# Kernel optimization log

Hardware: AMD Instinct MI355X
Metric: run time of the kernel (lower is better)

Reference implementation:

```python
import jax, jax.numpy as jnp
import numpy as np
import math

N_EMBD = 1024
N_HEAD = 16
HEAD_DIM = N_EMBD // N_HEAD


def setup_inputs() -> dict:
    key = jax.random.key(0)
    k_x, k_w1, k_b1, k_w2, k_b2 = jax.random.split(key, 5)
    B, T = 2, 2048
    x = jax.random.normal(k_x, (B, T, N_EMBD), dtype=jnp.float32)
    # ln1: Linear(n_embd, 3*n_embd); weights stored as [in, out] for x @ W
    W_qkv = jax.random.normal(k_w1, (N_EMBD, 3 * N_EMBD), dtype=jnp.float32) * 0.02
    b_qkv = jax.random.normal(k_b1, (3 * N_EMBD,), dtype=jnp.float32) * 0.02
    # ln2: Linear(n_embd, n_embd)
    W_out = jax.random.normal(k_w2, (N_EMBD, N_EMBD), dtype=jnp.float32) * 0.02
    b_out = jax.random.normal(k_b2, (N_EMBD,), dtype=jnp.float32) * 0.02
    return {"x": x, "W_qkv": W_qkv, "b_qkv": b_qkv, "W_out": W_out, "b_out": b_out}


def reference(x, W_qkv, b_qkv, W_out, b_out):
    B, T, C = x.shape
    qkv = x @ W_qkv + b_qkv                      # [B,T,3C]
    q, k, v = jnp.split(qkv, 3, axis=-1)
    # reshape to heads: [B, H, T, D]
    def to_heads(t):
        return t.reshape(B, T, N_HEAD, HEAD_DIM).transpose(0, 2, 1, 3)
    Q, K, V = to_heads(q), to_heads(k), to_heads(v)
    # NOTE: scale is 1/sqrt(n_head), as in the source (not sqrt(head_dim));
    # NOTE: no causal mask is applied, faithfully matching the source forward.
    scale = 1.0 / math.sqrt(N_HEAD)
    scores = jnp.einsum('bhqd,bhkd->bhqk', Q, K) * scale  # [B,H,T,T]
    attn = jax.nn.softmax(scores, axis=-1)
    out = jnp.einsum('bhqk,bhkd->bhqd', attn, V)          # [B,H,T,D]
    out = out.transpose(0, 2, 1, 3).reshape(B, T, C)
    # dropout = 0.0 -> identity (eval mode)
    return out @ W_out + b_out
```

## Files before the change

kernel.cpp:

```cpp
#include <hip/hip_runtime.h>
#include <hip/hip_bf16.h>
#include <stdint.h>

typedef __bf16 bf16_t;
typedef __bf16 bf16x8 __attribute__((ext_vector_type(8)));
typedef float  f32x4  __attribute__((ext_vector_type(4)));

#define AS1 __attribute__((address_space(1)))
#define AS3 __attribute__((address_space(3)))

__device__ __forceinline__ void gload16(const bf16_t* g, char* l) {
  __builtin_amdgcn_global_load_lds((AS1 const void*)(uintptr_t)g, (AS3 void*)l, 16, 0, 0);
}
__device__ __forceinline__ int swz8(int r) { return (r & 7) ^ ((r >> 2) & 6); }

#define C2S 0.36067376022224085f

__global__ __launch_bounds__(256) void prep(
    const float* __restrict__ x, const float* __restrict__ Wqkv, const float* __restrict__ Wout,
    bf16_t* __restrict__ xb, bf16_t* __restrict__ wqkvT, bf16_t* __restrict__ woutT) {
  __shared__ float tile[32][33];
  const int bid = blockIdx.x, tid = threadIdx.x;
  if (bid < 4096) {
    const int i = bid * 256 + tid;
    float4 v = reinterpret_cast<const float4*>(x)[i];
    union { bf16_t h[4]; unsigned long long u; } r;
    r.h[0] = (bf16_t)v.x; r.h[1] = (bf16_t)v.y; r.h[2] = (bf16_t)v.z; r.h[3] = (bf16_t)v.w;
    reinterpret_cast<unsigned long long*>(xb)[i] = r.u;
    return;
  }
  const float* W; bf16_t* Wt; int N, tb;
  if (bid < 7168) { W = Wqkv; Wt = wqkvT; N = 3072; tb = bid - 4096; }
  else            { W = Wout; Wt = woutT; N = 1024; tb = bid - 7168; }
  const int kb = (tb & 31) * 32, nb = (tb >> 5) * 32;
  const int tx = tid & 31, ty = tid >> 5;
#pragma unroll
  for (int i = 0; i < 32; i += 8)
    tile[ty + i][tx] = W[(size_t)(kb + ty + i) * N + nb + tx];
  __syncthreads();
  const int r = tid >> 3;
  const int c0 = (tid & 7) * 4;
  union { bf16_t h4[4]; unsigned long long u; } pk;
#pragma unroll
  for (int j = 0; j < 4; ++j) pk.h4[j] = (bf16_t)tile[c0 + j][r];
  *reinterpret_cast<unsigned long long*>(&Wt[(size_t)(nb + r) * 1024 + kb + c0]) = pk.u;
}

__global__ __launch_bounds__(512) void gemm8(
    const bf16_t* __restrict__ A, const bf16_t* __restrict__ Bt,
    const float* __restrict__ bias,
    bf16_t* __restrict__ outb, bf16_t* __restrict__ vtb,
    int N, int K, int ldo) {
  __shared__ bf16_t lA[3][4096];
  __shared__ bf16_t lB[3][4096];
  const int tid = threadIdx.x;
  const int wave = tid >> 6, lane = tid & 63;
  const int lr = lane & 15, lg = lane >> 4;
  const int ntiles = N >> 7;
  const int bid = (blockIdx.x & 7) * ((int)gridDim.x >> 3) + (blockIdx.x >> 3);
  const int bn = bid % ntiles, bm = bid / ntiles;
  const int m0 = bm * 128, n0 = bn * 128;
  const int wr = wave >> 2, wc = wave & 3;
  f32x4 acc[4][2] = {};

  const int srow = tid >> 2;
  const int scolb = ((tid & 3) << 4) ^ (((srow >> 1) & 3) << 4);
  const bf16_t* Asrc = A  + (size_t)(m0 + srow) * K + (scolb >> 1);
  const bf16_t* Bsrc = Bt + (size_t)(n0 + srow) * K + (scolb >> 1);
  auto stage = [&](int buf, int k0) {
    gload16(Asrc + k0, (char*)&lA[buf][0] + wave * 1024);
    gload16(Bsrc + k0, (char*)&lB[buf][0] + wave * 1024);
  };

  auto ldA = [&](const char* p, int mi) {
    const int row = wr * 64 + mi * 16 + lr;
    return *reinterpret_cast<const bf16x8*>(p + row * 64 + ((lg * 16) ^ (((row >> 1) & 3) << 4)));
  };
  auto ldB = [&](const char* p, int ni) {
    const int row = wc * 32 + ni * 16 + lr;
    return *reinterpret_cast<const bf16x8*>(p + row * 64 + ((lg * 16) ^ (((row >> 1) & 3) << 4)));
  };

  const int nt = K >> 5;
  stage(0, 0);
  stage(1, 32);
  int cur = 0, stg = 2;

  for (int t = 0; t < nt; ++t) {
    if (t + 2 < nt) {
      stage(stg, (t + 2) << 5);
      asm volatile("s_waitcnt vmcnt(4)" ::: "memory");
    } else if (t + 1 < nt) {
      asm volatile("s_waitcnt vmcnt(2)" ::: "memory");
    } else {
      asm volatile("s_waitcnt vmcnt(0)" ::: "memory");
    }
    __builtin_amdgcn_s_barrier();
    __builtin_amdgcn_sched_barrier(0);

    const char* pA = (const char*)&lA[cur][0];
    const char* pB = (const char*)&lB[cur][0];
    bf16x8 af[4], bfv[2];
#pragma unroll
    for (int mi = 0; mi < 4; ++mi) af[mi] = ldA(pA, mi);
    bfv[0] = ldB(pB, 0); bfv[1] = ldB(pB, 1);

    __builtin_amdgcn_s_setprio(1);
#pragma unroll
    for (int mi = 0; mi < 4; ++mi)
#pragma unroll
      for (int ni = 0; ni < 2; ++ni)
        acc[mi][ni] = __builtin_amdgcn_mfma_f32_16x16x32_bf16(af[mi], bfv[ni], acc[mi][ni], 0, 0, 0);
    __builtin_amdgcn_s_setprio(0);

    __builtin_amdgcn_sched_barrier(0);
    __builtin_amdgcn_s_barrier();
    cur = cur == 2 ? 0 : cur + 1;
    stg = stg == 2 ? 0 : stg + 1;
  }

#pragma unroll
  for (int mi = 0; mi < 4; ++mi) {
#pragma unroll
    for (int ni = 0; ni < 2; ++ni) {
      const int col = n0 + wc * 32 + ni * 16 + lr;
      const float bv = bias[col];
      const int rg0 = m0 + wr * 64 + mi * 16 + lg * 4;
      if (col >= 2048) {
        const int colv = col - 2048;
        const int dd = colv & 63, hh = colv >> 6;
        const int bb = rg0 >> 11, t = rg0 & 2047;
        union { bf16_t h4[4]; unsigned long long u; } pk;
#pragma unroll
        for (int r = 0; r < 4; ++r) pk.h4[r] = (bf16_t)(acc[mi][ni][r] + bv);
        *reinterpret_cast<unsigned long long*>(
            vtb + (size_t)(bb * 16 + hh) * 131072 + (size_t)dd * 2048 + t) = pk.u;
      } else {
        const float sc = (col < 1024) ? C2S : 1.f;
#pragma unroll
        for (int r = 0; r < 4; ++r) {
          const float v = (acc[mi][ni][r] + bv) * sc;
          outb[(size_t)(rg0 + r) * ldo + col] = (bf16_t)v;
        }
      }
    }
  }
}

__global__ __launch_bounds__(512) void attn_fwd(
    const bf16_t* __restrict__ qkv2,
    const bf16_t* __restrict__ vT,
    bf16_t* __restrict__ a0, bf16_t* __restrict__ a1,
    float* __restrict__ lbuf) {
  __shared__ bf16_t lds[3][8192];
  const int tid = threadIdx.x;
  const int wave = tid >> 6, lane = tid & 63;
  const int lr = lane & 15, lg = lane >> 4;
  const int id = blockIdx.x;
  const int xcd = id & 7, slot = id >> 3;
  const int bh = xcd * 4 + (slot & 3);
  const int rest = slot >> 2;
  const int qb = rest & 7, kvh = rest >> 3;
  const int b = bh >> 4, h = bh & 15;

  const int q0 = qb * 256 + wave * 32;
  const bf16_t* Qp = qkv2 + (size_t)(b * 2048 + q0) * 2048 + h * 64;
  bf16x8 qf[2][2];
#pragma unroll
  for (int hx = 0; hx < 2; ++hx) {
    qf[hx][0] = *reinterpret_cast<const bf16x8*>(Qp + (size_t)(hx * 16 + lr) * 2048 + lg * 8);
    qf[hx][1] = *reinterpret_cast<const bf16x8*>(Qp + (size_t)(hx * 16 + lr) * 2048 + 32 + lg * 8);
  }

  const int kr = tid >> 3;
  const int ks = (tid & 7) ^ swz8(kr);
  const bf16_t* Ksrc = qkv2 + (size_t)(b * 2048 + kvh * 1024 + kr) * 2048 + 1024 + h * 64 + ks * 8;
  const bf16_t* Vsrc = vT + (size_t)bh * 131072 + (size_t)kr * 2048 + kvh * 1024 + ks * 8;

  auto stage = [&](int buf, int kb) {
    char* base = (char*)&lds[buf][0] + wave * 1024;
    gload16(Ksrc + (size_t)kb * 131072, base);
    gload16(Vsrc + (size_t)kb * 64, base + 8192);
  };

  int kofs[4][2], vofs[4][2];
#pragma unroll
  for (int t = 0; t < 4; ++t) {
    const int kk = 32 * (t >> 1) + 8 * (lr >> 2) + 4 * (t & 1) + (lr & 3);
    const int sw = swz8(kk) << 4;
    kofs[t][0] = (kk << 7) + ((lg * 16) ^ sw);
    kofs[t][1] = (kk << 7) + ((64 + lg * 16) ^ sw);
  }
#pragma unroll
  for (int nc = 0; nc < 4; ++nc) {
    const int vr = nc * 16 + lr;
    const int sw = swz8(vr) << 4;
    vofs[nc][0] = 8192 + (vr << 7) + ((lg * 16) ^ sw);
    vofs[nc][1] = 8192 + (vr << 7) + ((64 + lg * 16) ^ sw);
  }

  f32x4 acc[2][4] = {};
  f32x4 accl[2] = {};
  bf16x8 ones;
#pragma unroll
  for (int j = 0; j < 8; ++j) ones[j] = (bf16_t)1.0f;

  stage(0, 0);
  stage(1, 1);
  int cur = 0, stg = 2;

  for (int kb = 0; kb < 16; ++kb) {
    if (kb + 2 < 16) stage(stg, kb + 2);
    if (kb + 2 < 16)      asm volatile("s_waitcnt vmcnt(4)" ::: "memory");
    else if (kb + 1 < 16) asm volatile("s_waitcnt vmcnt(2)" ::: "memory");
    else                  asm volatile("s_waitcnt vmcnt(0)" ::: "memory");
    __builtin_amdgcn_s_barrier();
    __builtin_amdgcn_sched_barrier(0);
    const char* bK = (const char*)&lds[cur][0];

    f32x4 s[2][4];
#pragma unroll
    for (int t = 0; t < 4; ++t) {
      const bf16x8 k0 = *reinterpret_cast<const bf16x8*>(bK + kofs[t][0]);
      const bf16x8 k1 = *reinterpret_cast<const bf16x8*>(bK + kofs[t][1]);
#pragma unroll
      for (int hx = 0; hx < 2; ++hx) {
        f32x4 z = {0.f, 0.f, 0.f, 0.f};
        z = __builtin_amdgcn_mfma_f32_16x16x32_bf16(k0, qf[hx][0], z, 0, 0, 0);
        s[hx][t] = __builtin_amdgcn_mfma_f32_16x16x32_bf16(k1, qf[hx][1], z, 0, 0, 0);
      }
    }

    bf16x8 pa[2][2];
#pragma unroll
    for (int hx = 0; hx < 2; ++hx) {
      float p[16];
#pragma unroll
      for (int t = 0; t < 4; ++t)
#pragma unroll
        for (int r = 0; r < 4; ++r)
          p[t * 4 + r] = __builtin_amdgcn_exp2f(s[hx][t][r]);
#pragma unroll
      for (int j = 0; j < 8; ++j) { pa[hx][0][j] = (bf16_t)p[j]; pa[hx][1][j] = (bf16_t)p[8 + j]; }
    }

    __builtin_amdgcn_s_setprio(1);
#pragma unroll
    for (int hx = 0; hx < 2; ++hx) {
      accl[hx] = __builtin_amdgcn_mfma_f32_16x16x32_bf16(pa[hx][0], ones, accl[hx], 0, 0, 0);
      accl[hx] = __builtin_amdgcn_mfma_f32_16x16x32_bf16(pa[hx][1], ones, accl[hx], 0, 0, 0);
    }
#pragma unroll
    for (int nc = 0; nc < 4; ++nc) {
      const bf16x8 v0 = *reinterpret_cast<const bf16x8*>(bK + vofs[nc][0]);
      const bf16x8 v1 = *reinterpret_cast<const bf16x8*>(bK + vofs[nc][1]);
#pragma unroll
      for (int hx = 0; hx < 2; ++hx) {
        acc[hx][nc] = __builtin_amdgcn_mfma_f32_16x16x32_bf16(pa[hx][0], v0, acc[hx][nc], 0, 0, 0);
        acc[hx][nc] = __builtin_amdgcn_mfma_f32_16x16x32_bf16(pa[hx][1], v1, acc[hx][nc], 0, 0, 0);
      }
    }
    __builtin_amdgcn_s_setprio(0);

    __builtin_amdgcn_sched_barrier(0);
    __builtin_amdgcn_s_barrier();
    cur = cur == 2 ? 0 : cur + 1;
    stg = stg == 2 ? 0 : stg + 1;
  }

  bf16_t* ap = kvh ? a1 : a0;
#pragma unroll
  for (int hx = 0; hx < 2; ++hx) {
#pragma unroll
    for (int r = 0; r < 4; ++r) {
      const float lf = 1.f / accl[hx][r];
      const int qg = q0 + hx * 16 + lg * 4 + r;
      bf16_t* op = ap + (size_t)(b * 2048 + qg) * 1024 + h * 64 + lr;
#pragma unroll
      for (int nc = 0; nc < 4; ++nc) op[nc * 16] = (bf16_t)(acc[hx][nc][r] * lf);
      if (lr == 0)
        lbuf[(size_t)(kvh * 4096 + b * 2048 + qg) * 16 + h] = accl[hx][r];
    }
  }
}

__global__ __launch_bounds__(256) void gemm2m(
    const bf16_t* __restrict__ a0, const bf16_t* __restrict__ a1,
    const float* __restrict__ lbuf, const bf16_t* __restrict__ Bt,
    const float* __restrict__ bias, float* __restrict__ outf) {
  __shared__ bf16_t lA[2][2048];
  __shared__ bf16_t lB[2][4096];
  const int tid = threadIdx.x;
  const int wave = tid >> 6, lane = tid & 63;
  const int lr = lane & 15, lg = lane >> 4;
  const int bid = (blockIdx.x & 7) * 64 + (blockIdx.x >> 3);
  const int bm = bid >> 3, bn = bid & 7;
  const int m0 = bm * 64, n0 = bn * 128;
  const int wr = wave >> 1, wc = wave & 1;
  f32x4 acc[2][4] = {};

  const int srow = tid >> 2;
  const int scolb = ((tid & 3) << 4) ^ (((srow >> 1) & 3) << 4);
  const int scol = scolb >> 1;

  const bf16_t* pa0 = a0 + (size_t)(m0 + srow) * 1024 + scol;
  const bf16_t* pa1 = a1 + (size_t)(m0 + srow) * 1024 + scol;
  const float*  pl0 = lbuf + (size_t)(m0 + srow) * 16;
  const float*  pl1 = lbuf + (size_t)(4096 + m0 + srow) * 16;
  const bf16_t* pB0 = Bt + (size_t)(n0 + srow) * 1024 + scol;
  const bf16_t* pB1 = Bt + (size_t)(n0 + 64 + srow) * 1024 + scol;

  bf16x8 nA0 = *reinterpret_cast<const bf16x8*>(pa0);
  bf16x8 nA1 = *reinterpret_cast<const bf16x8*>(pa1);
  float  nl0 = pl0[0], nl1 = pl1[0];
  bf16x8 nB0v = *reinterpret_cast<const bf16x8*>(pB0);
  bf16x8 nB1v = *reinterpret_cast<const bf16x8*>(pB1);

  for (int t = 0; t < 32; ++t) {
    const int cur = t & 1;
    const float inv = 1.f / (nl0 + nl1);
    const float w0 = nl0 * inv, w1 = nl1 * inv;
    bf16x8 mv;
#pragma unroll
    for (int j = 0; j < 8; ++j)
      mv[j] = (bf16_t)(w0 * (float)nA0[j] + w1 * (float)nA1[j]);
    *reinterpret_cast<bf16x8*>((char*)&lA[cur][0] + tid * 16) = mv;
    *reinterpret_cast<bf16x8*>((char*)&lB[cur][0] + tid * 16) = nB0v;
    *reinterpret_cast<bf16x8*>((char*)&lB[cur][0] + 4096 + tid * 16) = nB1v;
    __syncthreads();

    if (t < 31) {
      const int k0 = (t + 1) * 32;
      const int h = k0 >> 6;
      nA0 = *reinterpret_cast<const bf16x8*>(pa0 + k0);
      nA1 = *reinterpret_cast<const bf16x8*>(pa1 + k0);
      nl0 = pl0[h]; nl1 = pl1[h];
      nB0v = *reinterpret_cast<const bf16x8*>(pB0 + k0);
      nB1v = *reinterpret_cast<const bf16x8*>(pB1 + k0);
    }

    const char* pA = (const char*)&lA[cur][0];
    const char* pB = (const char*)&lB[cur][0];
    bf16x8 af[2], bfv[4];
#pragma unroll
    for (int mi = 0; mi < 2; ++mi) {
      const int row = wr * 32 + mi * 16 + lr;
      af[mi] = *reinterpret_cast<const bf16x8*>(pA + row * 64 + ((lg * 16) ^ (((row >> 1) & 3) << 4)));
    }
#pragma unroll
    for (int ni = 0; ni < 4; ++ni) {
      const int row = wc * 64 + ni * 16 + lr;
      bfv[ni] = *reinterpret_cast<const bf16x8*>(pB + row * 64 + ((lg * 16) ^ (((row >> 1) & 3) << 4)));
    }
    __builtin_amdgcn_s_setprio(1);
#pragma unroll
    for (int mi = 0; mi < 2; ++mi)
#pragma unroll
      for (int ni = 0; ni < 4; ++ni)
        acc[mi][ni] = __builtin_amdgcn_mfma_f32_16x16x32_bf16(af[mi], bfv[ni], acc[mi][ni], 0, 0, 0);
    __builtin_amdgcn_s_setprio(0);
    __syncthreads();
  }

#pragma unroll
  for (int mi = 0; mi < 2; ++mi)
#pragma unroll
    for (int ni = 0; ni < 4; ++ni) {
      const int col = n0 + wc * 64 + ni * 16 + lr;
      const float bv = bias[col];
      const int rg0 = m0 + wr * 32 + mi * 16 + lg * 4;
#pragma unroll
      for (int r = 0; r < 4; ++r)
        outf[(size_t)(rg0 + r) * 1024 + col] = acc[mi][ni][r] + bv;
    }
}

extern "C" void kernel_launch(void* const* d_in, const int* in_sizes, int n_in,
                              void* d_out, int out_size, void* d_ws, size_t ws_size,
                              hipStream_t stream) {
  (void)in_sizes; (void)n_in; (void)out_size; (void)ws_size;
  const float* x    = (const float*)d_in[0];
  const float* Wqkv = (const float*)d_in[1];
  const float* bqkv = (const float*)d_in[2];
  const float* Wout = (const float*)d_in[3];
  const float* bout = (const float*)d_in[4];
  float* out = (float*)d_out;

  char* ws = (char*)d_ws;
  bf16_t* xb    = (bf16_t*)(ws);
  bf16_t* a0    = (bf16_t*)(ws);
  bf16_t* wqkvT = (bf16_t*)(ws + 8388608);
  bf16_t* woutT = (bf16_t*)(ws + 14680064);
  bf16_t* qkv2  = (bf16_t*)(ws + 16777216);
  bf16_t* vT    = (bf16_t*)(ws + 33554432);
  bf16_t* a1    = (bf16_t*)(ws + 41943040);
  float*  lbuf  = (float*)(ws + 50331648);

  prep<<<8192, 256, 0, stream>>>(x, Wqkv, Wout, xb, wqkvT, woutT);
  gemm8<<<768, 512, 0, stream>>>(xb, wqkvT, bqkv, qkv2, vT, 3072, 1024, 2048);
  attn_fwd<<<512, 512, 0, stream>>>(qkv2, vT, a0, a1, lbuf);
  gemm2m<<<512, 256, 0, stream>>>(a0, a1, lbuf, woutT, bout, out);
}
```

Measured before the change: 112.3 us.

## Double per-wave query rows in attention and replace ones-MFMA row sums with VALU

The attention kernel now runs 4 waves per block, each handling 64 query rows instead of 32. This doubles reuse of each K/V fragment read from LDS per wave, and each thread stages two K and two V chunks. The row-sum denominator is now accumulated in VALU adds and reduced with cross-lane shuffles, replacing the extra MFMAs against a ones vector. The cost is higher register pressure from larger accumulators and fewer waves per block to hide latency.

```diff
diff --git a/kernel.cpp b/kernel.cpp
--- a/kernel.cpp
+++ b/kernel.cpp
@@ -147,7 +147,7 @@
   }
 }
 
-__global__ __launch_bounds__(512) void attn_fwd(
+__global__ __launch_bounds__(256) void attn_fwd(
     const bf16_t* __restrict__ qkv2,
     const bf16_t* __restrict__ vT,
     bf16_t* __restrict__ a0, bf16_t* __restrict__ a1,
@@ -163,24 +163,28 @@
   const int qb = rest & 7, kvh = rest >> 3;
   const int b = bh >> 4, h = bh & 15;
 
-  const int q0 = qb * 256 + wave * 32;
+  const int q0 = qb * 256 + wave * 64;
   const bf16_t* Qp = qkv2 + (size_t)(b * 2048 + q0) * 2048 + h * 64;
-  bf16x8 qf[2][2];
-#pragma unroll
-  for (int hx = 0; hx < 2; ++hx) {
+  bf16x8 qf[4][2];
+#pragma unroll
+  for (int hx = 0; hx < 4; ++hx) {
     qf[hx][0] = *reinterpret_cast<const bf16x8*>(Qp + (size_t)(hx * 16 + lr) * 2048 + lg * 8);
     qf[hx][1] = *reinterpret_cast<const bf16x8*>(Qp + (size_t)(hx * 16 + lr) * 2048 + 32 + lg * 8);
   }
 
-  const int kr = tid >> 3;
-  const int ks = (tid & 7) ^ swz8(kr);
-  const bf16_t* Ksrc = qkv2 + (size_t)(b * 2048 + kvh * 1024 + kr) * 2048 + 1024 + h * 64 + ks * 8;
-  const bf16_t* Vsrc = vT + (size_t)bh * 131072 + (size_t)kr * 2048 + kvh * 1024 + ks * 8;
+  const int kr0 = tid >> 3;
+  const int ks  = (tid & 7) ^ swz8(kr0);
+  const bf16_t* Ks0 = qkv2 + (size_t)(b * 2048 + kvh * 1024 + kr0) * 2048 + 1024 + h * 64 + ks * 8;
+  const bf16_t* Ks1 = Ks0 + (size_t)32 * 2048;
+  const bf16_t* Vs0 = vT + (size_t)bh * 131072 + (size_t)kr0 * 2048 + kvh * 1024 + ks * 8;
+  const bf16_t* Vs1 = Vs0 + (size_t)32 * 2048;
 
   auto stage = [&](int buf, int kb) {
     char* base = (char*)&lds[buf][0] + wave * 1024;
-    gload16(Ksrc + (size_t)kb * 131072, base);
-    gload16(Vsrc + (size_t)kb * 64, base + 8192);
+    gload16(Ks0 + (size_t)kb * 131072, base);
+    gload16(Ks1 + (size_t)kb * 131072, base + 4096);
+    gload16(Vs0 + (size_t)kb * 64, base + 8192);
+    gload16(Vs1 + (size_t)kb * 64, base + 12288);
   };
 
   int kofs[4][2], vofs[4][2];
@@ -199,63 +203,61 @@
     vofs[nc][1] = 8192 + (vr << 7) + ((64 + lg * 16) ^ sw);
   }
 
-  f32x4 acc[2][4] = {};
-  f32x4 accl[2] = {};
-  bf16x8 ones;
-#pragma unroll
-  for (int j = 0; j < 8; ++j) ones[j] = (bf16_t)1.0f;
+  f32x4 acc[4][4] = {};
+  f32x4 lac[4] = {};
 
   stage(0, 0);
   stage(1, 1);
   int cur = 0, stg = 2;
 
   for (int kb = 0; kb < 16; ++kb) {
-    if (kb + 2 < 16) stage(stg, kb + 2);
-    if (kb + 2 < 16)      asm volatile("s_waitcnt vmcnt(4)" ::: "memory");
-    else if (kb + 1 < 16) asm volatile("s_waitcnt vmcnt(2)" ::: "memory");
-    else                  asm volatile("s_waitcnt vmcnt(0)" ::: "memory");
+    if (kb + 2 < 16) {
+      stage(stg, kb + 2);
+      asm volatile("s_waitcnt vmcnt(8)" ::: "memory");
+    } else if (kb + 1 < 16) {
+      asm volatile("s_waitcnt vmcnt(4)" ::: "memory");
+    } else {
+      asm volatile("s_waitcnt vmcnt(0)" ::: "memory");
+    }
     __builtin_amdgcn_s_barrier();
     __builtin_amdgcn_sched_barrier(0);
     const char* bK = (const char*)&lds[cur][0];
 
-    f32x4 s[2][4];
+    f32x4 s[4][4];
 #pragma unroll
     for (int t = 0; t < 4; ++t) {
       const bf16x8 k0 = *reinterpret_cast<const bf16x8*>(bK + kofs[t][0]);
       const bf16x8 k1 = *reinterpret_cast<const bf16x8*>(bK + kofs[t][1]);
 #pragma unroll
-      for (int hx = 0; hx < 2; ++hx) {
+      for (int hx = 0; hx < 4; ++hx) {
         f32x4 z = {0.f, 0.f, 0.f, 0.f};
         z = __builtin_amdgcn_mfma_f32_16x16x32_bf16(k0, qf[hx][0], z, 0, 0, 0);
         s[hx][t] = __builtin_amdgcn_mfma_f32_16x16x32_bf16(k1, qf[hx][1], z, 0, 0, 0);
       }
     }
 
-    bf16x8 pa[2][2];
-#pragma unroll
-    for (int hx = 0; hx < 2; ++hx) {
+    bf16x8 pa[4][2];
+#pragma unroll
+    for (int hx = 0; hx < 4; ++hx) {
       float p[16];
 #pragma unroll
       for (int t = 0; t < 4; ++t)
 #pragma unroll
-        for (int r = 0; r < 4; ++r)
+        for (int r = 0; r < 4; ++r) {
           p[t * 4 + r] = __builtin_amdgcn_exp2f(s[hx][t][r]);
+          lac[hx][r] += p[t * 4 + r];
+        }
 #pragma unroll
       for (int j = 0; j < 8; ++j) { pa[hx][0][j] = (bf16_t)p[j]; pa[hx][1][j] = (bf16_t)p[8 + j]; }
     }
 
     __builtin_amdgcn_s_setprio(1);
-#pragma unroll
-    for (int hx = 0; hx < 2; ++hx) {
-      accl[hx] = __builtin_amdgcn_mfma_f32_16x16x32_bf16(pa[hx][0], ones, accl[hx], 0, 0, 0);
-      accl[hx] = __builtin_amdgcn_mfma_f32_16x16x32_bf16(pa[hx][1], ones, accl[hx], 0, 0, 0);
-    }
 #pragma unroll
     for (int nc = 0; nc < 4; ++nc) {
       const bf16x8 v0 = *reinterpret_cast<const bf16x8*>(bK + vofs[nc][0]);
       const bf16x8 v1 = *reinterpret_cast<const bf16x8*>(bK + vofs[nc][1]);
 #pragma unroll
-      for (int hx = 0; hx < 2; ++hx) {
+      for (int hx = 0; hx < 4; ++hx) {
         acc[hx][nc] = __builtin_amdgcn_mfma_f32_16x16x32_bf16(pa[hx][0], v0, acc[hx][nc], 0, 0, 0);
         acc[hx][nc] = __builtin_amdgcn_mfma_f32_16x16x32_bf16(pa[hx][1], v1, acc[hx][nc], 0, 0, 0);
       }
@@ -270,17 +272,21 @@
 
   bf16_t* ap = kvh ? a1 : a0;
 #pragma unroll
-  for (int hx = 0; hx < 2; ++hx) {
+  for (int hx = 0; hx < 4; ++hx) {
+    float lsum = (lac[hx][0] + lac[hx][1]) + (lac[hx][2] + lac[hx][3]);
+    lsum += __shfl_xor(lsum, 16);
+    lsum += __shfl_xor(lsum, 32);
+    const float li = 1.f / lsum;
 #pragma unroll
     for (int r = 0; r < 4; ++r) {
-      const float lf = 1.f / accl[hx][r];
+      const float lf = __shfl(li, lg * 4 + r);
       const int qg = q0 + hx * 16 + lg * 4 + r;
       bf16_t* op = ap + (size_t)(b * 2048 + qg) * 1024 + h * 64 + lr;
 #pragma unroll
       for (int nc = 0; nc < 4; ++nc) op[nc * 16] = (bf16_t)(acc[hx][nc][r] * lf);
-      if (lr == 0)
-        lbuf[(size_t)(kvh * 4096 + b * 2048 + qg) * 16 + h] = accl[hx][r];
-    }
+    }
+    if (lane < 16)
+      lbuf[(size_t)(kvh * 4096 + b * 2048 + q0 + hx * 16 + lane) * 16 + h] = lsum;
   }
 }
 
@@ -398,6 +404,6 @@
 
   prep<<<8192, 256, 0, stream>>>(x, Wqkv, Wout, xb, wqkvT, woutT);
   gemm8<<<768, 512, 0, stream>>>(xb, wqkvT, bqkv, qkv2, vT, 3072, 1024, 2048);
-  attn_fwd<<<512, 512, 0, stream>>>(qkv2, vT, a0, a1, lbuf);
+  attn_fwd<<<512, 256, 0, stream>>>(qkv2, vT, a0, a1, lbuf);
   gemm2m<<<512, 256, 0, stream>>>(a0, a1, lbuf, woutT, bout, out);
 }
```

Result: slower. 120.3 us (+7.2%).
